# Performance work log

Measured on AMD Instinct MI355X. Metric: run time of the kernel, lower is better.

## Reference

```python
import jax, jax.numpy as jnp
import numpy as np

N_SUBJECTS = 16
N_LABELS = 8
DENS_TEMP = 0.1  # args.ProtoSim_dens_temp


def setup_inputs() -> dict:
    key = jax.random.key(0)
    k1, k2, k3 = jax.random.split(key, 3)
    B, C, D = 16384, 2, 1024
    X_data = jax.random.normal(k1, (B, C, D), dtype=jnp.float32)
    subject = jax.random.randint(k2, (B,), 0, N_SUBJECTS, dtype=jnp.int64) if jax.config.jax_enable_x64 else jax.random.randint(k2, (B,), 0, N_SUBJECTS).astype(jnp.int32)
    labels = jax.random.randint(k3, (B,), 0, N_LABELS).astype(subject.dtype)
    return {"X_data": X_data, "subject": subject, "labels": labels}


def reference(X_data, subject, labels):
    B, C, D = X_data.shape
    K = N_SUBJECTS * N_LABELS  # all (subject,label) groups assumed present
    # contrast_feature = cat(unbind(X_data, 1), 0) -> [B*C, D]
    feat = X_data.swapaxes(0, 1).reshape(B * C, D)
    sub2 = jnp.tile(subject, C)          # cat((subject, subject))
    lab2 = jnp.tile(labels, C)
    # torch.unique sorts -> group g = subject * N_LABELS + label matches loop order
    gid = sub2 * N_LABELS + lab2
    counts = jax.ops.segment_sum(jnp.ones((B * C,), feat.dtype), gid, num_segments=K)  # (K,)
    centroid = jax.ops.segment_sum(feat, gid, num_segments=K) / counts[:, None]       # (K, D)
    # per-row euclidean distance to own group centroid (torch.cdist to 1 point)
    dist = jnp.linalg.norm(feat - centroid[gid], axis=1)                               # (B*C,)
    mean_sqrt = jax.ops.segment_sum(jnp.sqrt(dist), gid, num_segments=K) / counts
    density = mean_sqrt / jnp.log(counts + 10.0)
    density = jnp.where(counts <= 1.0, density.max(), density)
    density = jnp.clip(density, jnp.quantile(density, 0.1), jnp.quantile(density, 0.9))
    density = DENS_TEMP * density / density.mean()                                     # (K,)
    # masks: positives = same label, different subject
    g_sub = jnp.arange(K) // N_LABELS
    g_lab = jnp.arange(K) % N_LABELS
    subj_mask = (sub2[:, None] != g_sub[None, :]).astype(feat.dtype)  # (B*C, K)
    lab_mask = (lab2[:, None] == g_lab[None, :]).astype(feat.dtype)
    mask = subj_mask * lab_mask
    # every row has N_SUBJECTS-1 positives (all groups present), so no row filtering
    sim = (feat @ centroid.T) / density[None, :]                                        # (B*C, K)
    sim = sim - sim.max(axis=1, keepdims=True)
    pos = sim * mask
    logp = jax.nn.log_softmax(pos, axis=1)
    row_loss = -(mask * logp).sum(axis=1) / mask.sum(axis=1)  # soft-target CE / #pos
    return row_loss.reshape(C, B).mean()
```

## Files before the change

### kernel.cpp

```cpp
#include <hip/hip_runtime.h>
#include <hip/hip_bf16.h>
#include <math.h>

#define NSUB 16
#define NLAB 8
#define KG 128
#define BN 16384
#define DD 1024

typedef float v4f __attribute__((ext_vector_type(4)));
typedef short short8v __attribute__((ext_vector_type(8)));

static __device__ __forceinline__ short f2bf(float f) {
    unsigned u = __builtin_bit_cast(unsigned, f);
    unsigned r = (u + 0x7fffu + ((u >> 16) & 1u)) >> 16;
    return (short)r;
}

static __device__ __forceinline__ short8v pack_bf8(float4 lo, float4 hi) {
    union { short8v s; __hip_bfloat162 h[4]; } u;
    u.h[0] = __float22bfloat162_rn(float2{lo.x, lo.y});
    u.h[1] = __float22bfloat162_rn(float2{lo.z, lo.w});
    u.h[2] = __float22bfloat162_rn(float2{hi.x, hi.y});
    u.h[3] = __float22bfloat162_rn(float2{hi.z, hi.w});
    return u.s;
}

static __device__ __forceinline__ float dot4(float4 v) {
    return v.x * v.x + v.y * v.y + v.z * v.z + v.w * v.w;
}

__global__ __launch_bounds__(1024) void k0_gid(const int* __restrict__ subject,
                                               const int* __restrict__ labels,
                                               int* __restrict__ gid, int* __restrict__ cnt) {
    __shared__ int h[KG];
    int t = threadIdx.x;
    if (t < KG) h[t] = 0;
    __syncthreads();
    int b = blockIdx.x * 1024 + t;
    int g = subject[b] * NLAB + labels[b];
    gid[b] = g;
    atomicAdd(&h[g], 1);
    __syncthreads();
    if (t < KG && h[t]) atomicAdd(&cnt[t], h[t]);
}

__global__ void k0b_offs(const int* __restrict__ cnt, int* __restrict__ offs,
                         int* __restrict__ cursor) {
    __shared__ int c[KG];
    int t = threadIdx.x;
    c[t] = cnt[t];
    __syncthreads();
    int o = 0;
    for (int j = 0; j < t; ++j) o += c[j];
    offs[t] = o;
    cursor[t] = o;
}

__global__ __launch_bounds__(1024) void k0c_scatter(const int* __restrict__ gid,
                                                    int* __restrict__ cursor,
                                                    int* __restrict__ rowlist) {
    __shared__ int lcnt[KG], lbase[KG], lcur[KG];
    int t = threadIdx.x;
    if (t < KG) { lcnt[t] = 0; lcur[t] = 0; }
    __syncthreads();
    int b = blockIdx.x * 1024 + t;
    int g = gid[b];
    atomicAdd(&lcnt[g], 1);
    __syncthreads();
    if (t < KG) lbase[t] = lcnt[t] ? atomicAdd(&cursor[t], lcnt[t]) : 0;
    __syncthreads();
    int pos = lbase[g] + atomicAdd(&lcur[g], 1);
    rowlist[pos] = b;
}

__global__ __launch_bounds__(256) void k1_centroid(const float* __restrict__ X,
                                                   const int* __restrict__ rowlist,
                                                   const int* __restrict__ offs,
                                                   const int* __restrict__ cnt,
                                                   float* __restrict__ centroid) {
    int g = blockIdx.x >> 2;
    int dq = blockIdx.x & 3;
    int d = dq * 256 + threadIdx.x;
    __shared__ int rows[512];
    int n = cnt[g], o = offs[g];
    if (n > 512) n = 512;
    for (int i = threadIdx.x; i < n; i += 256) rows[i] = rowlist[o + i];
    __syncthreads();
    float acc = 0.f;
    int i = 0;
    for (; i + 8 <= n; i += 8) {
        float v[16];
#pragma unroll
        for (int u = 0; u < 8; ++u) {
            size_t base = (size_t)rows[i + u] * 2048 + d;
            v[2 * u] = X[base];
            v[2 * u + 1] = X[base + 1024];
        }
#pragma unroll
        for (int u = 0; u < 16; ++u) acc += v[u];
    }
    for (; i < n; ++i) {
        size_t base = (size_t)rows[i] * 2048 + d;
        acc += X[base] + X[base + 1024];
    }
    centroid[(size_t)g * DD + d] = acc / (2.f * (float)n);
}

__global__ __launch_bounds__(256) void k2b_cbf(const float* __restrict__ centroid,
                                               unsigned short* __restrict__ Cbf,
                                               float* __restrict__ cnorm) {
    __shared__ float wsum[4];
    int g = blockIdx.x, t = threadIdx.x;
    float4 v = *(const float4*)(centroid + (size_t)g * DD + t * 4);
    short4 bv = make_short4(f2bf(v.x), f2bf(v.y), f2bf(v.z), f2bf(v.w));
    *(short4*)(Cbf + (size_t)g * DD + t * 4) = bv;
    float s = dot4(v);
#pragma unroll
    for (int x = 32; x; x >>= 1) s += __shfl_xor(s, x, 64);
    int lane = t & 63, w = t >> 6;
    if (lane == 0) wsum[w] = s;
    __syncthreads();
    if (t == 0) cnorm[g] = wsum[0] + wsum[1] + wsum[2] + wsum[3];
}

__global__ __launch_bounds__(256) void k5a_dot(const float* __restrict__ X,
                                               const unsigned short* __restrict__ Cbf,
                                               float* __restrict__ Dot,
                                               float* __restrict__ rownorm) {
    int t = threadIdx.x, lane = t & 63;
    int gw = blockIdx.x * 4 + (t >> 6);
    int row0 = gw * 32;
    int m = lane & 15, q = lane >> 4;
    int r0 = row0 + m, r1 = row0 + 16 + m;
    const float* a0p = X + (size_t)(r0 & (BN - 1)) * 2048 + (size_t)(r0 >> 14) * 1024 + q * 8;
    const float* a1p = X + (size_t)(r1 & (BN - 1)) * 2048 + (size_t)(r1 >> 14) * 1024 + q * 8;
    const unsigned short* bp = Cbf + (size_t)m * DD + q * 8;

    v4f acc[2][8];
#pragma unroll
    for (int i = 0; i < 2; ++i)
#pragma unroll
        for (int j = 0; j < 8; ++j) acc[i][j] = (v4f){0.f, 0.f, 0.f, 0.f};

    float s0 = 0.f, s1 = 0.f;
    float4 a0l = *(const float4*)(a0p), a0h = *(const float4*)(a0p + 4);
    float4 a1l = *(const float4*)(a1p), a1h = *(const float4*)(a1p + 4);
    s0 += dot4(a0l) + dot4(a0h);
    s1 += dot4(a1l) + dot4(a1h);
    short8v cb[8];
#pragma unroll
    for (int gt = 0; gt < 8; ++gt) cb[gt] = *(const short8v*)(bp + gt * 16 * DD);
    short8v ca0 = pack_bf8(a0l, a0h), ca1 = pack_bf8(a1l, a1h);

    for (int kc = 0; kc < 31; ++kc) {
        int k = (kc + 1) * 32;
        float4 na0l = *(const float4*)(a0p + k), na0h = *(const float4*)(a0p + k + 4);
        float4 na1l = *(const float4*)(a1p + k), na1h = *(const float4*)(a1p + k + 4);
        short8v nb[8];
#pragma unroll
        for (int gt = 0; gt < 8; ++gt) nb[gt] = *(const short8v*)(bp + gt * 16 * DD + k);
#pragma unroll
        for (int gt = 0; gt < 8; ++gt) {
            acc[0][gt] = __builtin_amdgcn_mfma_f32_16x16x32_bf16(ca0, cb[gt], acc[0][gt], 0, 0, 0);
            acc[1][gt] = __builtin_amdgcn_mfma_f32_16x16x32_bf16(ca1, cb[gt], acc[1][gt], 0, 0, 0);
        }
        s0 += dot4(na0l) + dot4(na0h);
        s1 += dot4(na1l) + dot4(na1h);
        ca0 = pack_bf8(na0l, na0h);
        ca1 = pack_bf8(na1l, na1h);
#pragma unroll
        for (int gt = 0; gt < 8; ++gt) cb[gt] = nb[gt];
    }
#pragma unroll
    for (int gt = 0; gt < 8; ++gt) {
        acc[0][gt] = __builtin_amdgcn_mfma_f32_16x16x32_bf16(ca0, cb[gt], acc[0][gt], 0, 0, 0);
        acc[1][gt] = __builtin_amdgcn_mfma_f32_16x16x32_bf16(ca1, cb[gt], acc[1][gt], 0, 0, 0);
    }

    s0 += __shfl_xor(s0, 16, 64); s0 += __shfl_xor(s0, 32, 64);
    s1 += __shfl_xor(s1, 16, 64); s1 += __shfl_xor(s1, 32, 64);
    if (lane < 16) rownorm[r0] = s0;
    else if (lane < 32) rownorm[r1] = s1;

#pragma unroll
    for (int tile = 0; tile < 2; ++tile)
#pragma unroll
        for (int reg = 0; reg < 4; ++reg) {
            int row = row0 + tile * 16 + q * 4 + reg;
#pragma unroll
            for (int gt = 0; gt < 8; ++gt)
                Dot[(size_t)row * KG + gt * 16 + m] = acc[tile][gt][reg];
        }
}

__global__ __launch_bounds__(1024) void k3b_dist(const float* __restrict__ Dot,
                                                 const float* __restrict__ rownorm,
                                                 const float* __restrict__ cnorm,
                                                 const int* __restrict__ gid,
                                                 float* __restrict__ sqrtsum) {
    __shared__ float h[KG];
    int t = threadIdx.x;
    if (t < KG) h[t] = 0.f;
    __syncthreads();
    int r = blockIdx.x * 1024 + t;
    int b = r & (BN - 1);
    int g = gid[b];
    float d2 = rownorm[r] - 2.f * Dot[(size_t)r * KG + g] + cnorm[g];
    d2 = fmaxf(d2, 0.f);
    atomicAdd(&h[g], sqrtf(sqrtf(d2)));
    __syncthreads();
    if (t < KG && h[t] != 0.f) atomicAdd(&sqrtsum[t], h[t]);
}

__global__ void k4_density(const float* __restrict__ sqrtsum,
                           const int* __restrict__ cnt,
                           float* __restrict__ recipDen) {
    __shared__ float tmp[KG];
    __shared__ float d1s[KG];
    __shared__ float qv[4];
    int g = threadIdx.x;
    float cntf = 2.f * (float)cnt[g];
    float d0 = (sqrtsum[g] / cntf) / logf(cntf + 10.f);
    tmp[g] = d0;
    __syncthreads();
    float dmax = -INFINITY;
    for (int j = 0; j < KG; ++j) dmax = fmaxf(dmax, tmp[j]);
    float v = (cntf <= 1.f) ? dmax : d0;
    d1s[g] = v;
    __syncthreads();
    int less = 0, eq = 0;
    for (int j = 0; j < KG; ++j) {
        float u = d1s[j];
        less += (u < v) ? 1 : 0;
        eq += (u == v) ? 1 : 0;
    }
    const int ppos[4] = {12, 13, 114, 115};
    for (int q = 0; q < 4; ++q)
        if (less <= ppos[q] && ppos[q] < less + eq) qv[q] = v;
    __syncthreads();
    float q10 = 0.3f * qv[0] + 0.7f * qv[1];
    float q90 = 0.7f * qv[2] + 0.3f * qv[3];
    float d2 = fminf(fmaxf(v, q10), q90);
    __syncthreads();
    tmp[g] = d2;
    __syncthreads();
    float sum = 0.f;
    for (int j = 0; j < KG; ++j) sum += tmp[j];
    float mean = sum / (float)KG;
    float den = 0.1f * d2 / mean;
    recipDen[g] = 1.f / den;
}

__global__ __launch_bounds__(256) void k5b_loss(const float* __restrict__ Dot,
                                                const int* __restrict__ gid,
                                                const float* __restrict__ recipDen,
                                                float* __restrict__ out) {
    __shared__ float wsum[4];
    int t = threadIdx.x, lane = t & 63, w = t >> 6;
    int gwave = blockIdx.x * 4 + w;
    int g0 = lane, g1 = 64 + lane;
    float rd0 = recipDen[g0], rd1 = recipDen[g1];
    int s0g = g0 >> 3, l0g = g0 & 7, s1g = g1 >> 3, l1g = g1 & 7;
    float ll = 0.f;
    for (int i = 0; i < 32; ++i) {
        int row = gwave * 32 + i;
        int b = row & (BN - 1);
        int gb = gid[b];
        int s = gb >> 3, l = gb & 7;
        float sim0 = Dot[(size_t)row * KG + g0] * rd0;
        float sim1 = Dot[(size_t)row * KG + g1] * rd1;
        float mx = fmaxf(sim0, sim1);
#pragma unroll
        for (int x = 1; x < 64; x <<= 1) mx = fmaxf(mx, __shfl_xor(mx, x, 64));
        bool p0 = (l0g == l) && (s0g != s);
        bool p1 = (l1g == l) && (s1g != s);
        float S = 0.f, P = 0.f;
        if (p0) { float pv = sim0 - mx; S += expf(pv); P += pv; }
        if (p1) { float pv = sim1 - mx; S += expf(pv); P += pv; }
#pragma unroll
        for (int x = 1; x < 64; x <<= 1) { S += __shfl_xor(S, x, 64); P += __shfl_xor(P, x, 64); }
        if (lane == 0) ll += logf(113.f + S) - P * (1.f / 15.f);
    }
    if (lane == 0) wsum[w] = ll;
    __syncthreads();
    if (t == 0) atomicAdd(out, (wsum[0] + wsum[1] + wsum[2] + wsum[3]) * (1.f / 32768.f));
}

extern "C" void kernel_launch(void* const* d_in, const int* in_sizes, int n_in,
                              void* d_out, int out_size, void* d_ws, size_t ws_size,
                              hipStream_t stream) {
    const float* X = (const float*)d_in[0];
    const int* subject = (const int*)d_in[1];
    const int* labels = (const int*)d_in[2];
    float* out = (float*)d_out;
    char* w = (char*)d_ws;
    int* gid = (int*)(w + 0);
    int* cnt = (int*)(w + 65536);
    int* offs = (int*)(w + 66048);
    int* cursor = (int*)(w + 66560);
    float* sqrtsum = (float*)(w + 67072);
    float* recipDen = (float*)(w + 67584);
    float* cnorm = (float*)(w + 68096);
    int* rowlist = (int*)(w + 131072);
    float* centroid = (float*)(w + 262144);
    unsigned short* Cbf = (unsigned short*)(w + 786432);
    float* rownorm = (float*)(w + 1048576);
    float* Dot = (float*)(w + 2097152);

    hipMemsetAsync(cnt, 0, KG * sizeof(int), stream);
    hipMemsetAsync(sqrtsum, 0, KG * sizeof(float), stream);
    hipMemsetAsync(out, 0, sizeof(float), stream);

    k0_gid<<<16, 1024, 0, stream>>>(subject, labels, gid, cnt);
    k0b_offs<<<1, KG, 0, stream>>>(cnt, offs, cursor);
    k0c_scatter<<<16, 1024, 0, stream>>>(gid, cursor, rowlist);
    k1_centroid<<<KG * 4, 256, 0, stream>>>(X, rowlist, offs, cnt, centroid);
    k2b_cbf<<<KG, 256, 0, stream>>>(centroid, Cbf, cnorm);
    k5a_dot<<<256, 256, 0, stream>>>(X, Cbf, Dot, rownorm);
    k3b_dist<<<32, 1024, 0, stream>>>(Dot, rownorm, cnorm, gid, sqrtsum);
    k4_density<<<1, KG, 0, stream>>>(sqrtsum, cnt, recipDen);
    k5b_loss<<<256, 256, 0, stream>>>(Dot, gid, recipDen, out);
}
```

Before: 290.2 us.

## Fuse pipeline kernels and restructure dot and loss stages

Cuts the pipeline from nine launches to five. The offset prefix scan moves into the scatter kernel, and the bf16 conversion and centroid norm move into the centroid kernel, with partial norms combined by atomics. The per-row distance and sqrt-sum now run in the MFMA dot kernel's epilogue, and the density computation is redone inside every loss block. The dot kernel gets a two-stage software pipeline for its loads, and the loss kernel switches from one wave per row to one thread per row. These changes remove launch gaps and a re-read of Dot and rownorm, at the cost of redundant density work in each block and more register pressure in the dot kernel.

```diff
diff --git a/kernel.cpp b/kernel.cpp
--- a/kernel.cpp
+++ b/kernel.cpp
@@ -45,47 +45,51 @@
     if (t < KG && h[t]) atomicAdd(&cnt[t], h[t]);
 }
 
-__global__ void k0b_offs(const int* __restrict__ cnt, int* __restrict__ offs,
-                         int* __restrict__ cursor) {
-    __shared__ int c[KG];
-    int t = threadIdx.x;
-    c[t] = cnt[t];
-    __syncthreads();
-    int o = 0;
-    for (int j = 0; j < t; ++j) o += c[j];
-    offs[t] = o;
-    cursor[t] = o;
-}
-
 __global__ __launch_bounds__(1024) void k0c_scatter(const int* __restrict__ gid,
+                                                    const int* __restrict__ cnt,
                                                     int* __restrict__ cursor,
                                                     int* __restrict__ rowlist) {
-    __shared__ int lcnt[KG], lbase[KG], lcur[KG];
+    __shared__ int cval[KG], coff[KG], lcnt[KG], lbase[KG], lcur[KG];
     int t = threadIdx.x;
-    if (t < KG) { lcnt[t] = 0; lcur[t] = 0; }
-    __syncthreads();
+    if (t < KG) { cval[t] = cnt[t]; lcnt[t] = 0; lcur[t] = 0; }
+    __syncthreads();
+    if (t < KG) {
+        int o = 0;
+        for (int j = 0; j < t; ++j) o += cval[j];
+        coff[t] = o;
+    }
     int b = blockIdx.x * 1024 + t;
     int g = gid[b];
     atomicAdd(&lcnt[g], 1);
     __syncthreads();
-    if (t < KG) lbase[t] = lcnt[t] ? atomicAdd(&cursor[t], lcnt[t]) : 0;
-    __syncthreads();
-    int pos = lbase[g] + atomicAdd(&lcur[g], 1);
-    rowlist[pos] = b;
+    if (t < KG) lbase[t] = coff[t] + (lcnt[t] ? atomicAdd(&cursor[t], lcnt[t]) : 0);
+    __syncthreads();
+    rowlist[lbase[g] + atomicAdd(&lcur[g], 1)] = b;
 }
 
 __global__ __launch_bounds__(256) void k1_centroid(const float* __restrict__ X,
                                                    const int* __restrict__ rowlist,
-                                                   const int* __restrict__ offs,
                                                    const int* __restrict__ cnt,
-                                                   float* __restrict__ centroid) {
+                                                   unsigned short* __restrict__ Cbf,
+                                                   float* __restrict__ cnorm) {
     int g = blockIdx.x >> 2;
     int dq = blockIdx.x & 3;
-    int d = dq * 256 + threadIdx.x;
+    int t = threadIdx.x, d = dq * 256 + t;
+    int lane = t & 63, w = t >> 6;
     __shared__ int rows[512];
-    int n = cnt[g], o = offs[g];
-    if (n > 512) n = 512;
-    for (int i = threadIdx.x; i < n; i += 256) rows[i] = rowlist[o + i];
+    __shared__ int sh_no[2];
+    __shared__ float wsum[4];
+    if (w == 0) {
+        int v = 0;
+        if (lane < g) v += cnt[lane];
+        if (lane + 64 < g) v += cnt[lane + 64];
+#pragma unroll
+        for (int x = 32; x; x >>= 1) v += __shfl_xor(v, x, 64);
+        if (lane == 0) { sh_no[0] = v; sh_no[1] = cnt[g]; }
+    }
+    __syncthreads();
+    int o = sh_no[0], n = min(sh_no[1], 512);
+    for (int i = t; i < n; i += 256) rows[i] = rowlist[o + i];
     __syncthreads();
     float acc = 0.f;
     int i = 0;
@@ -104,31 +108,26 @@
         size_t base = (size_t)rows[i] * 2048 + d;
         acc += X[base] + X[base + 1024];
     }
-    centroid[(size_t)g * DD + d] = acc / (2.f * (float)n);
-}
-
-__global__ __launch_bounds__(256) void k2b_cbf(const float* __restrict__ centroid,
-                                               unsigned short* __restrict__ Cbf,
-                                               float* __restrict__ cnorm) {
-    __shared__ float wsum[4];
-    int g = blockIdx.x, t = threadIdx.x;
-    float4 v = *(const float4*)(centroid + (size_t)g * DD + t * 4);
-    short4 bv = make_short4(f2bf(v.x), f2bf(v.y), f2bf(v.z), f2bf(v.w));
-    *(short4*)(Cbf + (size_t)g * DD + t * 4) = bv;
-    float s = dot4(v);
+    float c = acc / (2.f * (float)n);
+    Cbf[(size_t)g * DD + d] = (unsigned short)f2bf(c);
+    float s = c * c;
 #pragma unroll
     for (int x = 32; x; x >>= 1) s += __shfl_xor(s, x, 64);
-    int lane = t & 63, w = t >> 6;
     if (lane == 0) wsum[w] = s;
     __syncthreads();
-    if (t == 0) cnorm[g] = wsum[0] + wsum[1] + wsum[2] + wsum[3];
+    if (t == 0) atomicAdd(&cnorm[g], wsum[0] + wsum[1] + wsum[2] + wsum[3]);
 }
 
 __global__ __launch_bounds__(256) void k5a_dot(const float* __restrict__ X,
                                                const unsigned short* __restrict__ Cbf,
+                                               const int* __restrict__ gid,
+                                               const float* __restrict__ cnorm,
                                                float* __restrict__ Dot,
-                                               float* __restrict__ rownorm) {
+                                               float* __restrict__ sqrtsum) {
+    __shared__ float h[KG];
     int t = threadIdx.x, lane = t & 63;
+    if (t < KG) h[t] = 0.f;
+    __syncthreads();
     int gw = blockIdx.x * 4 + (t >> 6);
     int row0 = gw * 32;
     int m = lane & 15, q = lane >> 4;
@@ -144,144 +143,177 @@
         for (int j = 0; j < 8; ++j) acc[i][j] = (v4f){0.f, 0.f, 0.f, 0.f};
 
     float s0 = 0.f, s1 = 0.f;
-    float4 a0l = *(const float4*)(a0p), a0h = *(const float4*)(a0p + 4);
-    float4 a1l = *(const float4*)(a1p), a1h = *(const float4*)(a1p + 4);
-    s0 += dot4(a0l) + dot4(a0h);
-    s1 += dot4(a1l) + dot4(a1h);
-    short8v cb[8];
-#pragma unroll
-    for (int gt = 0; gt < 8; ++gt) cb[gt] = *(const short8v*)(bp + gt * 16 * DD);
-    short8v ca0 = pack_bf8(a0l, a0h), ca1 = pack_bf8(a1l, a1h);
-
-    for (int kc = 0; kc < 31; ++kc) {
-        int k = (kc + 1) * 32;
-        float4 na0l = *(const float4*)(a0p + k), na0h = *(const float4*)(a0p + k + 4);
-        float4 na1l = *(const float4*)(a1p + k), na1h = *(const float4*)(a1p + k + 4);
-        short8v nb[8];
-#pragma unroll
-        for (int gt = 0; gt < 8; ++gt) nb[gt] = *(const short8v*)(bp + gt * 16 * DD + k);
+    short8v caA0, caA1, caB0, caB1, cbA[8], cbB[8];
+    {
+        float4 t0l = *(const float4*)(a0p), t0h = *(const float4*)(a0p + 4);
+        float4 t1l = *(const float4*)(a1p), t1h = *(const float4*)(a1p + 4);
+        s0 += dot4(t0l) + dot4(t0h); s1 += dot4(t1l) + dot4(t1h);
+        caA0 = pack_bf8(t0l, t0h); caA1 = pack_bf8(t1l, t1h);
+        float4 u0l = *(const float4*)(a0p + 32), u0h = *(const float4*)(a0p + 36);
+        float4 u1l = *(const float4*)(a1p + 32), u1h = *(const float4*)(a1p + 36);
+        s0 += dot4(u0l) + dot4(u0h); s1 += dot4(u1l) + dot4(u1h);
+        caB0 = pack_bf8(u0l, u0h); caB1 = pack_bf8(u1l, u1h);
 #pragma unroll
         for (int gt = 0; gt < 8; ++gt) {
-            acc[0][gt] = __builtin_amdgcn_mfma_f32_16x16x32_bf16(ca0, cb[gt], acc[0][gt], 0, 0, 0);
-            acc[1][gt] = __builtin_amdgcn_mfma_f32_16x16x32_bf16(ca1, cb[gt], acc[1][gt], 0, 0, 0);
-        }
-        s0 += dot4(na0l) + dot4(na0h);
-        s1 += dot4(na1l) + dot4(na1h);
-        ca0 = pack_bf8(na0l, na0h);
-        ca1 = pack_bf8(na1l, na1h);
-#pragma unroll
-        for (int gt = 0; gt < 8; ++gt) cb[gt] = nb[gt];
-    }
-#pragma unroll
-    for (int gt = 0; gt < 8; ++gt) {
-        acc[0][gt] = __builtin_amdgcn_mfma_f32_16x16x32_bf16(ca0, cb[gt], acc[0][gt], 0, 0, 0);
-        acc[1][gt] = __builtin_amdgcn_mfma_f32_16x16x32_bf16(ca1, cb[gt], acc[1][gt], 0, 0, 0);
+            cbA[gt] = *(const short8v*)(bp + gt * 16 * DD);
+            cbB[gt] = *(const short8v*)(bp + gt * 16 * DD + 32);
+        }
+    }
+    float4 pA0l = *(const float4*)(a0p + 64), pA0h = *(const float4*)(a0p + 68);
+    float4 pA1l = *(const float4*)(a1p + 64), pA1h = *(const float4*)(a1p + 68);
+    float4 pB0l = *(const float4*)(a0p + 96), pB0h = *(const float4*)(a0p + 100);
+    float4 pB1l = *(const float4*)(a1p + 96), pB1h = *(const float4*)(a1p + 100);
+
+    for (int kc = 0; kc < 32; kc += 2) {
+        {
+            int kb = (kc + 2 <= 31 ? kc + 2 : 31) * 32;
+            short8v nb[8];
+#pragma unroll
+            for (int gt = 0; gt < 8; ++gt) nb[gt] = *(const short8v*)(bp + gt * 16 * DD + kb);
+#pragma unroll
+            for (int gt = 0; gt < 8; ++gt) {
+                acc[0][gt] = __builtin_amdgcn_mfma_f32_16x16x32_bf16(caA0, cbA[gt], acc[0][gt], 0, 0, 0);
+                acc[1][gt] = __builtin_amdgcn_mfma_f32_16x16x32_bf16(caA1, cbA[gt], acc[1][gt], 0, 0, 0);
+            }
+            if (kc < 30) {
+                s0 += dot4(pA0l) + dot4(pA0h); s1 += dot4(pA1l) + dot4(pA1h);
+                caA0 = pack_bf8(pA0l, pA0h); caA1 = pack_bf8(pA1l, pA1h);
+                int kf = (kc + 4 <= 31 ? kc + 4 : 0) * 32;
+                pA0l = *(const float4*)(a0p + kf); pA0h = *(const float4*)(a0p + kf + 4);
+                pA1l = *(const float4*)(a1p + kf); pA1h = *(const float4*)(a1p + kf + 4);
+            }
+#pragma unroll
+            for (int gt = 0; gt < 8; ++gt) cbA[gt] = nb[gt];
+        }
+        {
+            int kb = (kc + 3 <= 31 ? kc + 3 : 31) * 32;
+            short8v nb[8];
+#pragma unroll
+            for (int gt = 0; gt < 8; ++gt) nb[gt] = *(const short8v*)(bp + gt * 16 * DD + kb);
+#pragma unroll
+            for (int gt = 0; gt < 8; ++gt) {
+                acc[0][gt] = __builtin_amdgcn_mfma_f32_16x16x32_bf16(caB0, cbB[gt], acc[0][gt], 0, 0, 0);
+                acc[1][gt] = __builtin_amdgcn_mfma_f32_16x16x32_bf16(caB1, cbB[gt], acc[1][gt], 0, 0, 0);
+            }
+            if (kc < 30) {
+                s0 += dot4(pB0l) + dot4(pB0h); s1 += dot4(pB1l) + dot4(pB1h);
+                caB0 = pack_bf8(pB0l, pB0h); caB1 = pack_bf8(pB1l, pB1h);
+                int kf = (kc + 5 <= 31 ? kc + 5 : 0) * 32;
+                pB0l = *(const float4*)(a0p + kf); pB0h = *(const float4*)(a0p + kf + 4);
+                pB1l = *(const float4*)(a1p + kf); pB1h = *(const float4*)(a1p + kf + 4);
+            }
+#pragma unroll
+            for (int gt = 0; gt < 8; ++gt) cbB[gt] = nb[gt];
+        }
     }
 
     s0 += __shfl_xor(s0, 16, 64); s0 += __shfl_xor(s0, 32, 64);
     s1 += __shfl_xor(s1, 16, 64); s1 += __shfl_xor(s1, 32, 64);
-    if (lane < 16) rownorm[r0] = s0;
-    else if (lane < 32) rownorm[r1] = s1;
 
 #pragma unroll
     for (int tile = 0; tile < 2; ++tile)
 #pragma unroll
         for (int reg = 0; reg < 4; ++reg) {
             int row = row0 + tile * 16 + q * 4 + reg;
-#pragma unroll
-            for (int gt = 0; gt < 8; ++gt)
-                Dot[(size_t)row * KG + gt * 16 + m] = acc[tile][gt][reg];
-        }
-}
-
-__global__ __launch_bounds__(1024) void k3b_dist(const float* __restrict__ Dot,
-                                                 const float* __restrict__ rownorm,
-                                                 const float* __restrict__ cnorm,
-                                                 const int* __restrict__ gid,
-                                                 float* __restrict__ sqrtsum) {
-    __shared__ float h[KG];
-    int t = threadIdx.x;
-    if (t < KG) h[t] = 0.f;
-    __syncthreads();
-    int r = blockIdx.x * 1024 + t;
-    int b = r & (BN - 1);
-    int g = gid[b];
-    float d2 = rownorm[r] - 2.f * Dot[(size_t)r * KG + g] + cnorm[g];
-    d2 = fmaxf(d2, 0.f);
-    atomicAdd(&h[g], sqrtf(sqrtf(d2)));
+            int b = row & (BN - 1);
+            int g = gid[b];
+            float own = 0.f;
+#pragma unroll
+            for (int gt = 0; gt < 8; ++gt) {
+                float v = acc[tile][gt][reg];
+                Dot[(size_t)row * KG + gt * 16 + m] = v;
+                if ((g >> 4) == gt) own = v;
+            }
+            float rn = __shfl(tile ? s1 : s0, q * 4 + reg, 64);
+            if ((g & 15) == m) {
+                float d2 = fmaxf(rn - 2.f * own + cnorm[g], 0.f);
+                atomicAdd(&h[g], sqrtf(sqrtf(d2)));
+            }
+        }
     __syncthreads();
     if (t < KG && h[t] != 0.f) atomicAdd(&sqrtsum[t], h[t]);
-}
-
-__global__ void k4_density(const float* __restrict__ sqrtsum,
-                           const int* __restrict__ cnt,
-                           float* __restrict__ recipDen) {
-    __shared__ float tmp[KG];
-    __shared__ float d1s[KG];
-    __shared__ float qv[4];
-    int g = threadIdx.x;
-    float cntf = 2.f * (float)cnt[g];
-    float d0 = (sqrtsum[g] / cntf) / logf(cntf + 10.f);
-    tmp[g] = d0;
-    __syncthreads();
-    float dmax = -INFINITY;
-    for (int j = 0; j < KG; ++j) dmax = fmaxf(dmax, tmp[j]);
-    float v = (cntf <= 1.f) ? dmax : d0;
-    d1s[g] = v;
-    __syncthreads();
-    int less = 0, eq = 0;
-    for (int j = 0; j < KG; ++j) {
-        float u = d1s[j];
-        less += (u < v) ? 1 : 0;
-        eq += (u == v) ? 1 : 0;
-    }
-    const int ppos[4] = {12, 13, 114, 115};
-    for (int q = 0; q < 4; ++q)
-        if (less <= ppos[q] && ppos[q] < less + eq) qv[q] = v;
-    __syncthreads();
-    float q10 = 0.3f * qv[0] + 0.7f * qv[1];
-    float q90 = 0.7f * qv[2] + 0.3f * qv[3];
-    float d2 = fminf(fmaxf(v, q10), q90);
-    __syncthreads();
-    tmp[g] = d2;
-    __syncthreads();
-    float sum = 0.f;
-    for (int j = 0; j < KG; ++j) sum += tmp[j];
-    float mean = sum / (float)KG;
-    float den = 0.1f * d2 / mean;
-    recipDen[g] = 1.f / den;
 }
 
 __global__ __launch_bounds__(256) void k5b_loss(const float* __restrict__ Dot,
                                                 const int* __restrict__ gid,
-                                                const float* __restrict__ recipDen,
+                                                const float* __restrict__ sqrtsum,
+                                                const int* __restrict__ cnt,
                                                 float* __restrict__ out) {
+    __shared__ float tmp[KG], d1s[KG], qv[4];
+    __shared__ float recipDen[KG];
     __shared__ float wsum[4];
-    int t = threadIdx.x, lane = t & 63, w = t >> 6;
-    int gwave = blockIdx.x * 4 + w;
-    int g0 = lane, g1 = 64 + lane;
-    float rd0 = recipDen[g0], rd1 = recipDen[g1];
-    int s0g = g0 >> 3, l0g = g0 & 7, s1g = g1 >> 3, l1g = g1 & 7;
-    float ll = 0.f;
-    for (int i = 0; i < 32; ++i) {
-        int row = gwave * 32 + i;
-        int b = row & (BN - 1);
-        int gb = gid[b];
-        int s = gb >> 3, l = gb & 7;
-        float sim0 = Dot[(size_t)row * KG + g0] * rd0;
-        float sim1 = Dot[(size_t)row * KG + g1] * rd1;
-        float mx = fmaxf(sim0, sim1);
-#pragma unroll
-        for (int x = 1; x < 64; x <<= 1) mx = fmaxf(mx, __shfl_xor(mx, x, 64));
-        bool p0 = (l0g == l) && (s0g != s);
-        bool p1 = (l1g == l) && (s1g != s);
-        float S = 0.f, P = 0.f;
-        if (p0) { float pv = sim0 - mx; S += expf(pv); P += pv; }
-        if (p1) { float pv = sim1 - mx; S += expf(pv); P += pv; }
-#pragma unroll
-        for (int x = 1; x < 64; x <<= 1) { S += __shfl_xor(S, x, 64); P += __shfl_xor(P, x, 64); }
-        if (lane == 0) ll += logf(113.f + S) - P * (1.f / 15.f);
-    }
+    int t = threadIdx.x;
+    float cntf = 0.f, d0 = 0.f, v = 0.f;
+    if (t < KG) {
+        cntf = 2.f * (float)cnt[t];
+        d0 = (sqrtsum[t] / cntf) / logf(cntf + 10.f);
+        tmp[t] = d0;
+    }
+    __syncthreads();
+    if (t < KG) {
+        float dmax = -INFINITY;
+        for (int j = 0; j < KG; ++j) dmax = fmaxf(dmax, tmp[j]);
+        v = (cntf <= 1.f) ? dmax : d0;
+        d1s[t] = v;
+    }
+    __syncthreads();
+    if (t < KG) {
+        int less = 0, eq = 0;
+        for (int j = 0; j < KG; ++j) {
+            float u = d1s[j];
+            less += (u < v) ? 1 : 0;
+            eq += (u == v) ? 1 : 0;
+        }
+        const int ppos[4] = {12, 13, 114, 115};
+        for (int qq = 0; qq < 4; ++qq)
+            if (less <= ppos[qq] && ppos[qq] < less + eq) qv[qq] = v;
+    }
+    __syncthreads();
+    if (t < KG) {
+        float q10 = 0.3f * qv[0] + 0.7f * qv[1];
+        float q90 = 0.7f * qv[2] + 0.3f * qv[3];
+        tmp[t] = fminf(fmaxf(v, q10), q90);
+    }
+    __syncthreads();
+    if (t < KG) {
+        float sum = 0.f;
+        for (int j = 0; j < KG; ++j) sum += tmp[j];
+        float mean = sum / (float)KG;
+        recipDen[t] = mean / (0.1f * tmp[t]);
+    }
+    __syncthreads();
+    int row = blockIdx.x * 256 + t;
+    int b = row & (BN - 1);
+    int g = gid[b];
+    int s = g >> 3, l = g & 7;
+    int lp = (l >> 2) & 1, lc = l & 3;
+    const float4* dp = (const float4*)(Dot + (size_t)row * KG);
+    float mx = -INFINITY;
+    float psave[16];
+#pragma unroll
+    for (int c = 0; c < 32; ++c) {
+        float4 dv = dp[c];
+        float4 rv = *(const float4*)&recipDen[c * 4];
+        float x0 = dv.x * rv.x, x1 = dv.y * rv.y, x2 = dv.z * rv.z, x3 = dv.w * rv.w;
+        mx = fmaxf(mx, fmaxf(fmaxf(x0, x1), fmaxf(x2, x3)));
+        if ((c & 1) == lp) {
+            float sel = (lc == 0) ? x0 : (lc == 1) ? x1 : (lc == 2) ? x2 : x3;
+            psave[c >> 1] = sel;
+        }
+    }
+    float S = 0.f, P = 0.f;
+#pragma unroll
+    for (int j = 0; j < 16; ++j) {
+        float pv = psave[j] - mx;
+        float e = expf(pv);
+        bool use = (j != s);
+        S += use ? e : 0.f;
+        P += use ? pv : 0.f;
+    }
+    float ll = logf(113.f + S) - P * (1.f / 15.f);
+#pragma unroll
+    for (int x = 32; x; x >>= 1) ll += __shfl_xor(ll, x, 64);
+    int lane = t & 63, w = t >> 6;
     if (lane == 0) wsum[w] = ll;
     __syncthreads();
     if (t == 0) atomicAdd(out, (wsum[0] + wsum[1] + wsum[2] + wsum[3]) * (1.f / 32768.f));
@@ -297,28 +329,19 @@
     char* w = (char*)d_ws;
     int* gid = (int*)(w + 0);
     int* cnt = (int*)(w + 65536);
-    int* offs = (int*)(w + 66048);
-    int* cursor = (int*)(w + 66560);
-    float* sqrtsum = (float*)(w + 67072);
-    float* recipDen = (float*)(w + 67584);
-    float* cnorm = (float*)(w + 68096);
+    float* sqrtsum = (float*)(w + 66048);
+    float* cnorm = (float*)(w + 66560);
+    int* cursor = (int*)(w + 67072);
     int* rowlist = (int*)(w + 131072);
-    float* centroid = (float*)(w + 262144);
-    unsigned short* Cbf = (unsigned short*)(w + 786432);
-    float* rownorm = (float*)(w + 1048576);
+    unsigned short* Cbf = (unsigned short*)(w + 262144);
     float* Dot = (float*)(w + 2097152);
 
-    hipMemsetAsync(cnt, 0, KG * sizeof(int), stream);
-    hipMemsetAsync(sqrtsum, 0, KG * sizeof(float), stream);
+    hipMemsetAsync(w + 65536, 0, 2048, stream);
     hipMemsetAsync(out, 0, sizeof(float), stream);
 
     k0_gid<<<16, 1024, 0, stream>>>(subject, labels, gid, cnt);
-    k0b_offs<<<1, KG, 0, stream>>>(cnt, offs, cursor);
-    k0c_scatter<<<16, 1024, 0, stream>>>(gid, cursor, rowlist);
-    k1_centroid<<<KG * 4, 256, 0, stream>>>(X, rowlist, offs, cnt, centroid);
-    k2b_cbf<<<KG, 256, 0, stream>>>(centroid, Cbf, cnorm);
-    k5a_dot<<<256, 256, 0, stream>>>(X, Cbf, Dot, rownorm);
-    k3b_dist<<<32, 1024, 0, stream>>>(Dot, rownorm, cnorm, gid, sqrtsum);
-    k4_density<<<1, KG, 0, stream>>>(sqrtsum, cnt, recipDen);
-    k5b_loss<<<256, 256, 0, stream>>>(Dot, gid, recipDen, out);
-}
+    k0c_scatter<<<16, 1024, 0, stream>>>(gid, cnt, cursor, rowlist);
+    k1_centroid<<<KG * 4, 256, 0, stream>>>(X, rowlist, cnt, Cbf, cnorm);
+    k5a_dot<<<256, 256, 0, stream>>>(X, Cbf, gid, cnorm, Dot, sqrtsum);
+    k5b_loss<<<128, 256, 0, stream>>>(Dot, gid, sqrtsum, cnt, out);
+}
```

Result: faster. 273.8 us (-5.6%).
